# Performance work log

Measured on AMD Instinct MI355X. Metric: run time of the kernel, lower is better.

## Reference

```python
import jax, jax.numpy as jnp
import numpy as np

D_MODEL = 1024
NHEAD = 16
HEAD_DIM = D_MODEL // NHEAD
B, T = 2, 2048


def setup_inputs() -> dict:
    key = jax.random.key(0)
    ks = jax.random.split(key, 12)
    s = 1.0 / np.sqrt(D_MODEL)
    return {
        "query": jax.random.normal(ks[0], (B, T, D_MODEL), jnp.float32),
        "key": jax.random.normal(ks[1], (B, T, D_MODEL), jnp.float32),
        "value": jax.random.normal(ks[2], (B, T, D_MODEL), jnp.float32),
        "key_padding_mask": jnp.zeros((B, T), dtype=bool),
        "attn_mask": jnp.zeros((T, T), jnp.float32),
        "stoich_frac": jax.random.uniform(ks[3], (B, T), jnp.float32),
        "Wq": jax.random.uniform(ks[4], (D_MODEL, D_MODEL), jnp.float32, -s, s),
        "bq": jnp.zeros((D_MODEL,), jnp.float32),
        "Wk": jax.random.uniform(ks[5], (D_MODEL, D_MODEL), jnp.float32, -s, s),
        "bk": jnp.zeros((D_MODEL,), jnp.float32),
        "Wv": jax.random.uniform(ks[6], (D_MODEL, D_MODEL), jnp.float32, -s, s),
        "bv": jnp.zeros((D_MODEL,), jnp.float32),
        "Wo": jax.random.uniform(ks[7], (D_MODEL, D_MODEL), jnp.float32, -s, s),
        "bo": jnp.zeros((D_MODEL,), jnp.float32),
        "stoich_alpha": jnp.float32(0.1),
    }


def reference(query, key, value, key_padding_mask, attn_mask, stoich_frac,
              Wq, bq, Wk, bk, Wv, bv, Wo, bo, stoich_alpha):
    Bq, Tq, _ = query.shape
    Tk = key.shape[1]
    scale = HEAD_DIM ** -0.5
    # Linear projections (torch Linear: x @ W.T + b), reshape to [B, H, T, Dh]
    Q = (query @ Wq.T + bq).reshape(Bq, Tq, NHEAD, HEAD_DIM).transpose(0, 2, 1, 3)
    K = (key @ Wk.T + bk).reshape(Bq, Tk, NHEAD, HEAD_DIM).transpose(0, 2, 1, 3)
    V = (value @ Wv.T + bv).reshape(Bq, Tk, NHEAD, HEAD_DIM).transpose(0, 2, 1, 3)
    # Scores [B, H, Tq, Tk]
    scores = jnp.einsum("bhqd,bhkd->bhqk", Q, K) * scale
    # Stoichiometric pairwise bias (T_q == T_k path)
    diff = stoich_frac[:, :, None] - stoich_frac[:, None, :]  # [B, Tq, Tk]
    bias = stoich_alpha * (jnp.log1p(jnp.abs(diff)) * jnp.sign(diff))
    scores = scores + bias[:, None, :, :]
    scores = scores + attn_mask  # broadcasts [Tq, Tk]
    scores = jnp.where(key_padding_mask[:, None, None, :], -jnp.inf, scores)
    probs = jax.nn.softmax(scores, axis=-1)
    # dropout: eval mode / p=0 -> identity
    out = jnp.einsum("bhqk,bhkd->bhqd", probs, V)
    out = out.transpose(0, 2, 1, 3).reshape(Bq, Tq, D_MODEL)
    return out @ Wo.T + bo
```

## Files before the change

kernel.cpp:

```cpp
#include <hip/hip_runtime.h>
#include <math.h>

typedef __bf16 bf16_t;
typedef __bf16 bf16x8 __attribute__((ext_vector_type(8)));
typedef __bf16 bf16x4 __attribute__((ext_vector_type(4)));
typedef float  f32x4  __attribute__((ext_vector_type(4)));

#define NHEAD 16
#define HDIM 64
#define DMODEL 1024
#define TSEQ 2048

#define SBAR() __builtin_amdgcn_s_barrier()
#define LGKM0() do { asm volatile("s_waitcnt lgkmcnt(0)" ::: "memory"); \
                     __builtin_amdgcn_sched_barrier(0); } while (0)

__device__ __forceinline__ f32x4 mfma16(bf16x8 a, bf16x8 b, f32x4 c) {
  return __builtin_amdgcn_mfma_f32_16x16x32_bf16(a, b, c, 0, 0, 0);
}

__device__ __forceinline__ void gload16(const bf16_t* g, bf16_t* l) {
  __builtin_amdgcn_global_load_lds((const __attribute__((address_space(1))) void*)g,
                                   (__attribute__((address_space(3))) void*)l, 16, 0, 0);
}

__device__ __forceinline__ unsigned pk2(float lo, float hi) {
  unsigned short a = __builtin_bit_cast(unsigned short, (__bf16)lo);
  unsigned short c = __builtin_bit_cast(unsigned short, (__bf16)hi);
  return ((unsigned)c << 16) | a;
}

__device__ __forceinline__ void cvtstore(f32x4 x0, f32x4 x1, bf16_t* dh, bf16_t* dl, int off) {
  bf16x8 hfr, lfr;
#pragma unroll
  for (int j = 0; j < 4; ++j) {
    float v = x0[j];
    __bf16 hb = (__bf16)v;
    hfr[j] = hb; lfr[j] = (__bf16)(v - (float)hb);
    float w = x1[j];
    __bf16 wb = (__bf16)w;
    hfr[4 + j] = wb; lfr[4 + j] = (__bf16)(w - (float)wb);
  }
  *(bf16x8*)(dh + off) = hfr;
  *(bf16x8*)(dl + off) = lfr;
}

__global__ __launch_bounds__(256)
void build_bias(const float* __restrict__ amask, const unsigned char* __restrict__ kpm,
                const float* __restrict__ sf, const float* __restrict__ alpha_p,
                bf16_t* __restrict__ BM) {
  size_t idx = (size_t)blockIdx.x * 256 + threadIdx.x;
  int k8 = (int)(idx & (TSEQ / 8 - 1));
  size_t bq = idx >> 8;
  int b = (int)(bq >> 11);
  int q = (int)(bq & (TSEQ - 1));
  const float sfq = sf[bq];
  const float alpha = *alpha_p;
  const float* sfk = sf + (size_t)b * TSEQ + k8 * 8;
  const float* am  = amask + (size_t)q * TSEQ + k8 * 8;
  const unsigned char* kp = kpm + (size_t)b * TSEQ + k8 * 8;
  bf16x8 o;
#pragma unroll
  for (int j = 0; j < 8; ++j) {
    float df = sfq - sfk[j];
    float v = alpha * copysignf(log1pf(fabsf(df)), df) + am[j];
    if (kp[j]) v = -1.0e30f;
    o[j] = (__bf16)v;
  }
  *(bf16x8*)&BM[idx * 8] = o;
}

template<int MODE>
__global__ __launch_bounds__(512)
void gemm_mfma(const float* __restrict__ A, const float* __restrict__ W,
               const float* __restrict__ bias,
               bf16_t* __restrict__ obh, bf16_t* __restrict__ obl,
               float* __restrict__ of) {
  __shared__ bf16_t AH[8 * 512], AL[8 * 512], WH[4 * 512], WL[4 * 512];
  const int tid = threadIdx.x;
  const int lane = tid & 63;
  const int a15 = lane & 15, g = lane >> 4;
  const int wv = tid >> 6, wm = wv >> 1, wn = wv & 1;
  const int m0 = blockIdx.y * 128, n0 = blockIdx.x * 64;
  f32x4 acc[2][2] = {};

  const int t0 = tid >> 6, l0 = tid & 63;
  const float* pA0 = A + (size_t)(m0 + t0 * 16 + (l0 & 15)) * DMODEL + 8 * (l0 >> 4);
  const bool doW = (tid < 256);
  const int sW = tid & 255;
  const int tw = sW >> 6, lw = sW & 63;
  const float* pW = W + (size_t)(n0 + tw * 16 + (lw & 15)) * DMODEL + 8 * (lw >> 4);

  f32x4 rA0a = *(const f32x4*)pA0, rA0b = *(const f32x4*)(pA0 + 4);
  f32x4 rWa = {}, rWb = {};
  if (doW) { rWa = *(const f32x4*)pW; rWb = *(const f32x4*)(pW + 4); }

  for (int k0 = 0; k0 < DMODEL; k0 += 32) {
    SBAR();
    cvtstore(rA0a, rA0b, AH, AL, tid * 8);
    if (doW) cvtstore(rWa, rWb, WH, WL, sW * 8);
    __builtin_amdgcn_sched_barrier(0);
    if (k0 + 32 < DMODEL) {
      pA0 += 32;
      rA0a = *(const f32x4*)pA0; rA0b = *(const f32x4*)(pA0 + 4);
      if (doW) { pW += 32; rWa = *(const f32x4*)pW; rWb = *(const f32x4*)(pW + 4); }
    }
    LGKM0();
    SBAR();

    bf16x8 ah[2], al[2], wh[2], wl[2];
#pragma unroll
    for (int i = 0; i < 2; ++i) {
      ah[i] = *(const bf16x8*)&AH[(wm * 2 + i) * 512 + lane * 8];
      al[i] = *(const bf16x8*)&AL[(wm * 2 + i) * 512 + lane * 8];
      wh[i] = *(const bf16x8*)&WH[(wn * 2 + i) * 512 + lane * 8];
      wl[i] = *(const bf16x8*)&WL[(wn * 2 + i) * 512 + lane * 8];
    }
    __builtin_amdgcn_s_setprio(1);
    if (MODE == 2) {
#pragma unroll
      for (int i = 0; i < 2; ++i)
#pragma unroll
        for (int j = 0; j < 2; ++j) {
          acc[i][j] = mfma16(wh[i], ah[j], acc[i][j]);
          acc[i][j] = mfma16(wh[i], al[j], acc[i][j]);
          acc[i][j] = mfma16(wl[i], ah[j], acc[i][j]);
        }
    } else {
#pragma unroll
      for (int i = 0; i < 2; ++i)
#pragma unroll
        for (int j = 0; j < 2; ++j) {
          acc[i][j] = mfma16(ah[i], wh[j], acc[i][j]);
          acc[i][j] = mfma16(ah[i], wl[j], acc[i][j]);
          acc[i][j] = mfma16(al[i], wh[j], acc[i][j]);
        }
    }
    __builtin_amdgcn_s_setprio(0);
  }

  if (MODE == 0) {
#pragma unroll
    for (int i = 0; i < 2; ++i)
#pragma unroll
      for (int j = 0; j < 2; ++j) {
        int n = n0 + wn * 32 + j * 16 + a15;
        float bs = bias[n];
#pragma unroll
        for (int r = 0; r < 4; ++r) {
          int m = m0 + wm * 32 + i * 16 + 4 * g + r;
          of[(size_t)m * DMODEL + n] = acc[i][j][r] + bs;
        }
      }
  } else if (MODE == 1) {
#pragma unroll
    for (int i = 0; i < 2; ++i)
#pragma unroll
      for (int j = 0; j < 2; ++j) {
        int n = n0 + wn * 32 + j * 16 + a15;
        float bs = bias[n];
        int hh = n >> 6, d = n & 63;
#pragma unroll
        for (int r = 0; r < 4; ++r) {
          int m = m0 + wm * 32 + i * 16 + 4 * g + r;
          int bb = m >> 11, t = m & (TSEQ - 1);
          float v = acc[i][j][r] + bs;
          size_t o = (((size_t)(bb * NHEAD + hh)) * TSEQ + t) * HDIM + d;
          __bf16 hb = (__bf16)v;
          obh[o] = hb;
          obl[o] = (__bf16)(v - (float)hb);
        }
      }
  } else {
#pragma unroll
    for (int i = 0; i < 2; ++i)
#pragma unroll
      for (int j = 0; j < 2; ++j) {
        int m = m0 + wm * 32 + j * 16 + a15;
        int bb = m >> 11, t = m & (TSEQ - 1);
#pragma unroll
        for (int r = 0; r < 4; ++r) {
          int n = n0 + wn * 32 + i * 16 + 4 * g + r;
          float v = acc[i][j][r] + bias[n];
          int hh = n >> 6, d = n & 63;
          size_t o = (((size_t)(bb * NHEAD + hh)) * HDIM + d) * TSEQ + t;
          __bf16 hb = (__bf16)v;
          obh[o] = hb;
          obl[o] = (__bf16)(v - (float)hb);
        }
      }
  }
}

__global__ __launch_bounds__(512)
void attn_mfma(const bf16_t* __restrict__ Qhi, const bf16_t* __restrict__ Qlo,
               const bf16_t* __restrict__ Khi, const bf16_t* __restrict__ Klo,
               const bf16_t* __restrict__ Vth, const bf16_t* __restrict__ Vtl,
               const bf16_t* __restrict__ BMt, float* __restrict__ O) {
  __shared__ bf16_t KH[2][8 * 512], KL[2][8 * 512], VH[2][8 * 512], VL[2][8 * 512];
  __shared__ bf16_t PS[8 * 512];
  const int tid = threadIdx.x;
  const int lane = tid & 63, wv = tid >> 6;
  const int a15 = lane & 15, g = lane >> 4;
  const int b = blockIdx.z, h = blockIdx.y, q0 = blockIdx.x * 128;
  const int bh = b * NHEAD + h;
  const int qg = q0 + wv * 16 + a15;
  constexpr int NT = TSEQ / 64;

  const bf16_t* Qh_b = Qhi + ((size_t)bh * TSEQ + qg) * HDIM;
  const bf16_t* Ql_b = Qlo + ((size_t)bh * TSEQ + qg) * HDIM;
  const bf16_t* Kh_b = Khi + (size_t)bh * TSEQ * HDIM;
  const bf16_t* Kl_b = Klo + (size_t)bh * TSEQ * HDIM;
  const bf16_t* Vh_b = Vth + (size_t)bh * HDIM * TSEQ;
  const bf16_t* Vl_b = Vtl + (size_t)bh * HDIM * TSEQ;
  const bf16_t* bmrow = BMt + ((size_t)b * TSEQ + qg) * TSEQ;

  bf16x8 qh[2], ql[2];
  qh[0] = *(const bf16x8*)&Qh_b[8 * g];
  qh[1] = *(const bf16x8*)&Qh_b[32 + 8 * g];
  ql[0] = *(const bf16x8*)&Ql_b[8 * g];
  ql[1] = *(const bf16x8*)&Ql_b[32 + 8 * g];

  f32x4 aco[4] = {};
  float m_run = -3.0e38f, l_run = 0.f;
  bf16x4 bmv[4], bmn[4];

  const int ts = wv >> 1, ks = wv & 1;
  auto stage = [&](int k0, int buf) {
    size_t ko = (size_t)(k0 + 16 * ts + a15) * HDIM + 32 * ks + 8 * g;
    gload16(Kh_b + ko, &KH[buf][wv * 512]);
    gload16(Kl_b + ko, &KL[buf][wv * 512]);
    size_t vo = (size_t)(16 * ts + a15) * TSEQ + k0 + 32 * ks + 8 * g;
    gload16(Vh_b + vo, &VH[buf][wv * 512]);
    gload16(Vl_b + vo, &VL[buf][wv * 512]);
  };

#pragma unroll
  for (int mt = 0; mt < 4; ++mt) bmv[mt] = *(const bf16x4*)&bmrow[16 * mt + 4 * g];
  stage(0, 0);

  for (int t = 0; t < NT; ++t) {
    const int cur = t & 1;
    if (t + 1 < NT) {
      const int kn = (t + 1) * 64;
#pragma unroll
      for (int mt = 0; mt < 4; ++mt) bmn[mt] = *(const bf16x4*)&bmrow[kn + 16 * mt + 4 * g];
      stage(kn, cur ^ 1);
      asm volatile("s_waitcnt vmcnt(8)" ::: "memory");
    } else {
      asm volatile("s_waitcnt vmcnt(0)" ::: "memory");
    }
    __builtin_amdgcn_sched_barrier(0);
    SBAR();

    f32x4 s4[4];
    __builtin_amdgcn_s_setprio(1);
#pragma unroll
    for (int mt = 0; mt < 4; ++mt) {
      bf16x8 k0h = *(const bf16x8*)&KH[cur][(mt * 2 + 0) * 512 + lane * 8];
      bf16x8 k1h = *(const bf16x8*)&KH[cur][(mt * 2 + 1) * 512 + lane * 8];
      bf16x8 k0l = *(const bf16x8*)&KL[cur][(mt * 2 + 0) * 512 + lane * 8];
      bf16x8 k1l = *(const bf16x8*)&KL[cur][(mt * 2 + 1) * 512 + lane * 8];
      f32x4 sa = {};
      sa = mfma16(k0h, qh[0], sa);
      sa = mfma16(k1h, qh[1], sa);
      sa = mfma16(k0h, ql[0], sa);
      sa = mfma16(k1h, ql[1], sa);
      sa = mfma16(k0l, qh[0], sa);
      sa = mfma16(k1l, qh[1], sa);
      s4[mt] = sa;
    }
    __builtin_amdgcn_s_setprio(0);

#pragma unroll
    for (int mt = 0; mt < 4; ++mt)
#pragma unroll
      for (int r = 0; r < 4; ++r)
        s4[mt][r] = fmaf(s4[mt][r], 0.125f, (float)bmv[mt][r]);

    float tmax = -3.0e38f;
#pragma unroll
    for (int mt = 0; mt < 4; ++mt)
#pragma unroll
      for (int r = 0; r < 4; ++r) tmax = fmaxf(tmax, s4[mt][r]);
    tmax = fmaxf(tmax, __shfl_xor(tmax, 16));
    tmax = fmaxf(tmax, __shfl_xor(tmax, 32));
    if (!__all(tmax - m_run <= 8.0f)) {
      float mnew = fmaxf(m_run, tmax);
      float corr = __expf(m_run - mnew);
      l_run *= corr;
#pragma unroll
      for (int dt = 0; dt < 4; ++dt) aco[dt] *= corr;
      m_run = mnew;
    }
    float psum = 0.f;
    unsigned pk01[4], pk23[4];
#pragma unroll
    for (int mt = 0; mt < 4; ++mt) {
      float p0 = __expf(s4[mt][0] - m_run);
      float p1 = __expf(s4[mt][1] - m_run);
      float p2 = __expf(s4[mt][2] - m_run);
      float p3 = __expf(s4[mt][3] - m_run);
      psum += (p0 + p1) + (p2 + p3);
      pk01[mt] = pk2(p0, p1);
      pk23[mt] = pk2(p2, p3);
    }
    psum += __shfl_xor(psum, 16);
    psum += __shfl_xor(psum, 32);
    l_run += psum;

    const int psb = wv * 512 + a15 * 32;
    const int r3 = a15 & 3;
    __builtin_amdgcn_s_setprio(1);
#pragma unroll
    for (int kss = 0; kss < 2; ++kss) {
#pragma unroll
      for (int mh = 0; mh < 2; ++mh) {
        int mt = kss * 2 + mh;
        int phys = ((mh << 1) | (g >> 1)) ^ r3;
        uint2 w2;
        w2.x = pk01[mt];
        w2.y = pk23[mt];
        *(uint2*)&PS[psb + phys * 8 + (g & 1) * 4] = w2;
      }
      LGKM0();
      bf16x8 pf = *(const bf16x8*)&PS[psb + ((g ^ r3) << 3)];
#pragma unroll
      for (int dt = 0; dt < 4; ++dt) {
        bf16x8 vh = *(const bf16x8*)&VH[cur][(dt * 2 + kss) * 512 + lane * 8];
        bf16x8 vl = *(const bf16x8*)&VL[cur][(dt * 2 + kss) * 512 + lane * 8];
        aco[dt] = mfma16(vh, pf, aco[dt]);
        aco[dt] = mfma16(vl, pf, aco[dt]);
      }
    }
    __builtin_amdgcn_s_setprio(0);

    if (t + 1 < NT) {
#pragma unroll
      for (int mt = 0; mt < 4; ++mt) bmv[mt] = bmn[mt];
    }
    SBAR();
  }

  float inv = 1.0f / l_run;
#pragma unroll
  for (int dt = 0; dt < 4; ++dt) {
    f32x4 o = aco[dt] * inv;
    *(f32x4*)&O[((size_t)b * TSEQ + qg) * DMODEL + h * HDIM + dt * 16 + 4 * g] = o;
  }
}

extern "C" void kernel_launch(void* const* d_in, const int* in_sizes, int n_in,
                              void* d_out, int out_size, void* d_ws, size_t ws_size,
                              hipStream_t stream) {
  const float* query = (const float*)d_in[0];
  const float* key = (const float*)d_in[1];
  const float* value = (const float*)d_in[2];
  const unsigned char* kpm = (const unsigned char*)d_in[3];
  const float* amask = (const float*)d_in[4];
  const float* sf = (const float*)d_in[5];
  const float* Wq = (const float*)d_in[6];
  const float* bq = (const float*)d_in[7];
  const float* Wk = (const float*)d_in[8];
  const float* bk = (const float*)d_in[9];
  const float* Wv = (const float*)d_in[10];
  const float* bv = (const float*)d_in[11];
  const float* Wo = (const float*)d_in[12];
  const float* bo = (const float*)d_in[13];
  const float* alpha = (const float*)d_in[14];
  float* out = (float*)d_out;

  const size_t NEL = (size_t)2 * NHEAD * TSEQ * HDIM;
  bf16_t* p = (bf16_t*)d_ws;
  bf16_t* Qh = p;
  bf16_t* Ql = p + NEL;
  bf16_t* Kh = p + 2 * NEL;
  bf16_t* Kl = p + 3 * NEL;
  bf16_t* Vh = p + 4 * NEL;
  bf16_t* Vl = p + 5 * NEL;
  float* Oa = (float*)(p + 6 * NEL);
  bf16_t* BMt = (bf16_t*)(Oa + (size_t)4096 * DMODEL);

  build_bias<<<dim3(4096), dim3(256), 0, stream>>>(amask, kpm, sf, alpha, BMt);

  dim3 gg(16, 32), gb(512);
  gemm_mfma<1><<<gg, gb, 0, stream>>>(query, Wq, bq, Qh, Ql, nullptr);
  gemm_mfma<1><<<gg, gb, 0, stream>>>(key, Wk, bk, Kh, Kl, nullptr);
  gemm_mfma<2><<<gg, gb, 0, stream>>>(value, Wv, bv, Vh, Vl, nullptr);
  dim3 ga(TSEQ / 128, NHEAD, 2);
  attn_mfma<<<ga, dim3(512), 0, stream>>>(Qh, Ql, Kh, Kl, Vh, Vl, BMt, Oa);
  gemm_mfma<0><<<gg, gb, 0, stream>>>(Oa, Wo, bo, nullptr, nullptr, out);
}
```

Measured before the change: 338.7 us.

## Process two 16-row query tiles per wave in attention, halving block threads

The attention kernel moves from 8 waves with one 16-query tile each to 4 waves with two 16-query tiles each (A and B), still 128 queries per block. Each K/V fragment read from LDS now feeds twice the MFMA work, which cuts LDS traffic per FLOP, and each wave stages two chunks of K/V. The bias prefetch now happens after the softmax instead of being double-buffered at the loop top. In exchange, per-thread register pressure roughly doubles (two accumulator sets, two score sets, two Q fragments) and there are half as many waves to hide latency.

```diff
diff --git a/kernel.cpp b/kernel.cpp
--- a/kernel.cpp
+++ b/kernel.cpp
@@ -192,60 +192,72 @@
   }
 }
 
-__global__ __launch_bounds__(512)
+__global__ __launch_bounds__(256)
 void attn_mfma(const bf16_t* __restrict__ Qhi, const bf16_t* __restrict__ Qlo,
                const bf16_t* __restrict__ Khi, const bf16_t* __restrict__ Klo,
                const bf16_t* __restrict__ Vth, const bf16_t* __restrict__ Vtl,
                const bf16_t* __restrict__ BMt, float* __restrict__ O) {
   __shared__ bf16_t KH[2][8 * 512], KL[2][8 * 512], VH[2][8 * 512], VL[2][8 * 512];
-  __shared__ bf16_t PS[8 * 512];
+  __shared__ bf16_t PS[4 * 2 * 512];
   const int tid = threadIdx.x;
   const int lane = tid & 63, wv = tid >> 6;
   const int a15 = lane & 15, g = lane >> 4;
   const int b = blockIdx.z, h = blockIdx.y, q0 = blockIdx.x * 128;
   const int bh = b * NHEAD + h;
-  const int qg = q0 + wv * 16 + a15;
+  const int qgA = q0 + wv * 32 + a15;
   constexpr int NT = TSEQ / 64;
 
-  const bf16_t* Qh_b = Qhi + ((size_t)bh * TSEQ + qg) * HDIM;
-  const bf16_t* Ql_b = Qlo + ((size_t)bh * TSEQ + qg) * HDIM;
+  const bf16_t* QhA = Qhi + ((size_t)bh * TSEQ + qgA) * HDIM;
+  const bf16_t* QlA = Qlo + ((size_t)bh * TSEQ + qgA) * HDIM;
   const bf16_t* Kh_b = Khi + (size_t)bh * TSEQ * HDIM;
   const bf16_t* Kl_b = Klo + (size_t)bh * TSEQ * HDIM;
   const bf16_t* Vh_b = Vth + (size_t)bh * HDIM * TSEQ;
   const bf16_t* Vl_b = Vtl + (size_t)bh * HDIM * TSEQ;
-  const bf16_t* bmrow = BMt + ((size_t)b * TSEQ + qg) * TSEQ;
-
-  bf16x8 qh[2], ql[2];
-  qh[0] = *(const bf16x8*)&Qh_b[8 * g];
-  qh[1] = *(const bf16x8*)&Qh_b[32 + 8 * g];
-  ql[0] = *(const bf16x8*)&Ql_b[8 * g];
-  ql[1] = *(const bf16x8*)&Ql_b[32 + 8 * g];
-
-  f32x4 aco[4] = {};
-  float m_run = -3.0e38f, l_run = 0.f;
-  bf16x4 bmv[4], bmn[4];
-
-  const int ts = wv >> 1, ks = wv & 1;
+  const bf16_t* bmA = BMt + ((size_t)b * TSEQ + qgA) * TSEQ;
+  const bf16_t* bmB = bmA + (size_t)16 * TSEQ;
+
+  bf16x8 qhA[2], qlA[2], qhB[2], qlB[2];
+  qhA[0] = *(const bf16x8*)&QhA[8 * g];
+  qhA[1] = *(const bf16x8*)&QhA[32 + 8 * g];
+  qlA[0] = *(const bf16x8*)&QlA[8 * g];
+  qlA[1] = *(const bf16x8*)&QlA[32 + 8 * g];
+  qhB[0] = *(const bf16x8*)&QhA[16 * HDIM + 8 * g];
+  qhB[1] = *(const bf16x8*)&QhA[16 * HDIM + 32 + 8 * g];
+  qlB[0] = *(const bf16x8*)&QlA[16 * HDIM + 8 * g];
+  qlB[1] = *(const bf16x8*)&QlA[16 * HDIM + 32 + 8 * g];
+
+  f32x4 acoA[4] = {}, acoB[4] = {};
+  float mA = -3.0e38f, lA = 0.f, mB = -3.0e38f, lB = 0.f;
+  bf16x4 bmvA[4], bmvB[4];
+
   auto stage = [&](int k0, int buf) {
-    size_t ko = (size_t)(k0 + 16 * ts + a15) * HDIM + 32 * ks + 8 * g;
-    gload16(Kh_b + ko, &KH[buf][wv * 512]);
-    gload16(Kl_b + ko, &KL[buf][wv * 512]);
-    size_t vo = (size_t)(16 * ts + a15) * TSEQ + k0 + 32 * ks + 8 * g;
-    gload16(Vh_b + vo, &VH[buf][wv * 512]);
-    gload16(Vl_b + vo, &VL[buf][wv * 512]);
+#pragma unroll
+    for (int c = 0; c < 2; ++c) {
+      int sb = wv * 2 + c;
+      size_t ko = (size_t)(k0 + 16 * wv + a15) * HDIM + 32 * c + 8 * g;
+      gload16(Kh_b + ko, &KH[buf][sb * 512]);
+      gload16(Kl_b + ko, &KL[buf][sb * 512]);
+      size_t vo = (size_t)(16 * wv + a15) * TSEQ + k0 + 32 * c + 8 * g;
+      gload16(Vh_b + vo, &VH[buf][sb * 512]);
+      gload16(Vl_b + vo, &VL[buf][sb * 512]);
+    }
   };
 
 #pragma unroll
-  for (int mt = 0; mt < 4; ++mt) bmv[mt] = *(const bf16x4*)&bmrow[16 * mt + 4 * g];
+  for (int mt = 0; mt < 4; ++mt) {
+    bmvA[mt] = *(const bf16x4*)&bmA[16 * mt + 4 * g];
+    bmvB[mt] = *(const bf16x4*)&bmB[16 * mt + 4 * g];
+  }
   stage(0, 0);
+
+  const int psbA = (wv * 2 + 0) * 512 + a15 * 32;
+  const int psbB = (wv * 2 + 1) * 512 + a15 * 32;
+  const int r3 = a15 & 3;
 
   for (int t = 0; t < NT; ++t) {
     const int cur = t & 1;
     if (t + 1 < NT) {
-      const int kn = (t + 1) * 64;
-#pragma unroll
-      for (int mt = 0; mt < 4; ++mt) bmn[mt] = *(const bf16x4*)&bmrow[kn + 16 * mt + 4 * g];
-      stage(kn, cur ^ 1);
+      stage((t + 1) * 64, cur ^ 1);
       asm volatile("s_waitcnt vmcnt(8)" ::: "memory");
     } else {
       asm volatile("s_waitcnt vmcnt(0)" ::: "memory");
@@ -253,7 +265,7 @@
     __builtin_amdgcn_sched_barrier(0);
     SBAR();
 
-    f32x4 s4[4];
+    f32x4 s4a[4], s4b[4];
     __builtin_amdgcn_s_setprio(1);
 #pragma unroll
     for (int mt = 0; mt < 4; ++mt) {
@@ -262,13 +274,21 @@
       bf16x8 k0l = *(const bf16x8*)&KL[cur][(mt * 2 + 0) * 512 + lane * 8];
       bf16x8 k1l = *(const bf16x8*)&KL[cur][(mt * 2 + 1) * 512 + lane * 8];
       f32x4 sa = {};
-      sa = mfma16(k0h, qh[0], sa);
-      sa = mfma16(k1h, qh[1], sa);
-      sa = mfma16(k0h, ql[0], sa);
-      sa = mfma16(k1h, ql[1], sa);
-      sa = mfma16(k0l, qh[0], sa);
-      sa = mfma16(k1l, qh[1], sa);
-      s4[mt] = sa;
+      sa = mfma16(k0h, qhA[0], sa);
+      sa = mfma16(k1h, qhA[1], sa);
+      sa = mfma16(k0h, qlA[0], sa);
+      sa = mfma16(k1h, qlA[1], sa);
+      sa = mfma16(k0l, qhA[0], sa);
+      sa = mfma16(k1l, qhA[1], sa);
+      s4a[mt] = sa;
+      f32x4 sb_ = {};
+      sb_ = mfma16(k0h, qhB[0], sb_);
+      sb_ = mfma16(k1h, qhB[1], sb_);
+      sb_ = mfma16(k0h, qlB[0], sb_);
+      sb_ = mfma16(k1h, qlB[1], sb_);
+      sb_ = mfma16(k0l, qhB[0], sb_);
+      sb_ = mfma16(k1l, qhB[1], sb_);
+      s4b[mt] = sb_;
     }
     __builtin_amdgcn_s_setprio(0);
 
@@ -276,41 +296,83 @@
     for (int mt = 0; mt < 4; ++mt)
 #pragma unroll
       for (int r = 0; r < 4; ++r)
-        s4[mt][r] = fmaf(s4[mt][r], 0.125f, (float)bmv[mt][r]);
-
-    float tmax = -3.0e38f;
+        s4a[mt][r] = fmaf(s4a[mt][r], 0.125f, (float)bmvA[mt][r]);
+    float tmaxA = -3.0e38f;
 #pragma unroll
     for (int mt = 0; mt < 4; ++mt)
 #pragma unroll
-      for (int r = 0; r < 4; ++r) tmax = fmaxf(tmax, s4[mt][r]);
-    tmax = fmaxf(tmax, __shfl_xor(tmax, 16));
-    tmax = fmaxf(tmax, __shfl_xor(tmax, 32));
-    if (!__all(tmax - m_run <= 8.0f)) {
-      float mnew = fmaxf(m_run, tmax);
-      float corr = __expf(m_run - mnew);
-      l_run *= corr;
-#pragma unroll
-      for (int dt = 0; dt < 4; ++dt) aco[dt] *= corr;
-      m_run = mnew;
-    }
-    float psum = 0.f;
-    unsigned pk01[4], pk23[4];
+      for (int r = 0; r < 4; ++r) tmaxA = fmaxf(tmaxA, s4a[mt][r]);
+    tmaxA = fmaxf(tmaxA, __shfl_xor(tmaxA, 16));
+    tmaxA = fmaxf(tmaxA, __shfl_xor(tmaxA, 32));
+    if (!__all(tmaxA - mA <= 8.0f)) {
+      float mn = fmaxf(mA, tmaxA);
+      float corr = __expf(mA - mn);
+      lA *= corr;
+#pragma unroll
+      for (int dt = 0; dt < 4; ++dt) acoA[dt] *= corr;
+      mA = mn;
+    }
+    float psumA = 0.f;
+    unsigned pk01A[4], pk23A[4];
 #pragma unroll
     for (int mt = 0; mt < 4; ++mt) {
-      float p0 = __expf(s4[mt][0] - m_run);
-      float p1 = __expf(s4[mt][1] - m_run);
-      float p2 = __expf(s4[mt][2] - m_run);
-      float p3 = __expf(s4[mt][3] - m_run);
-      psum += (p0 + p1) + (p2 + p3);
-      pk01[mt] = pk2(p0, p1);
-      pk23[mt] = pk2(p2, p3);
-    }
-    psum += __shfl_xor(psum, 16);
-    psum += __shfl_xor(psum, 32);
-    l_run += psum;
-
-    const int psb = wv * 512 + a15 * 32;
-    const int r3 = a15 & 3;
+      float p0 = __expf(s4a[mt][0] - mA);
+      float p1 = __expf(s4a[mt][1] - mA);
+      float p2 = __expf(s4a[mt][2] - mA);
+      float p3 = __expf(s4a[mt][3] - mA);
+      psumA += (p0 + p1) + (p2 + p3);
+      pk01A[mt] = pk2(p0, p1);
+      pk23A[mt] = pk2(p2, p3);
+    }
+    psumA += __shfl_xor(psumA, 16);
+    psumA += __shfl_xor(psumA, 32);
+    lA += psumA;
+
+#pragma unroll
+    for (int mt = 0; mt < 4; ++mt)
+#pragma unroll
+      for (int r = 0; r < 4; ++r)
+        s4b[mt][r] = fmaf(s4b[mt][r], 0.125f, (float)bmvB[mt][r]);
+    float tmaxB = -3.0e38f;
+#pragma unroll
+    for (int mt = 0; mt < 4; ++mt)
+#pragma unroll
+      for (int r = 0; r < 4; ++r) tmaxB = fmaxf(tmaxB, s4b[mt][r]);
+    tmaxB = fmaxf(tmaxB, __shfl_xor(tmaxB, 16));
+    tmaxB = fmaxf(tmaxB, __shfl_xor(tmaxB, 32));
+    if (!__all(tmaxB - mB <= 8.0f)) {
+      float mn = fmaxf(mB, tmaxB);
+      float corr = __expf(mB - mn);
+      lB *= corr;
+#pragma unroll
+      for (int dt = 0; dt < 4; ++dt) acoB[dt] *= corr;
+      mB = mn;
+    }
+    float psumB = 0.f;
+    unsigned pk01B[4], pk23B[4];
+#pragma unroll
+    for (int mt = 0; mt < 4; ++mt) {
+      float p0 = __expf(s4b[mt][0] - mB);
+      float p1 = __expf(s4b[mt][1] - mB);
+      float p2 = __expf(s4b[mt][2] - mB);
+      float p3 = __expf(s4b[mt][3] - mB);
+      psumB += (p0 + p1) + (p2 + p3);
+      pk01B[mt] = pk2(p0, p1);
+      pk23B[mt] = pk2(p2, p3);
+    }
+    psumB += __shfl_xor(psumB, 16);
+    psumB += __shfl_xor(psumB, 32);
+    lB += psumB;
+
+    if (t + 1 < NT) {
+      const int kn = (t + 1) * 64;
+#pragma unroll
+      for (int mt = 0; mt < 4; ++mt) {
+        bmvA[mt] = *(const bf16x4*)&bmA[kn + 16 * mt + 4 * g];
+        bmvB[mt] = *(const bf16x4*)&bmB[kn + 16 * mt + 4 * g];
+      }
+    }
+
     __builtin_amdgcn_s_setprio(1);
 #pragma unroll
     for (int kss = 0; kss < 2; ++kss) {
@@ -318,35 +380,36 @@
       for (int mh = 0; mh < 2; ++mh) {
         int mt = kss * 2 + mh;
         int phys = ((mh << 1) | (g >> 1)) ^ r3;
-        uint2 w2;
-        w2.x = pk01[mt];
-        w2.y = pk23[mt];
-        *(uint2*)&PS[psb + phys * 8 + (g & 1) * 4] = w2;
+        uint2 wA; wA.x = pk01A[mt]; wA.y = pk23A[mt];
+        *(uint2*)&PS[psbA + phys * 8 + (g & 1) * 4] = wA;
+        uint2 wB; wB.x = pk01B[mt]; wB.y = pk23B[mt];
+        *(uint2*)&PS[psbB + phys * 8 + (g & 1) * 4] = wB;
       }
       LGKM0();
-      bf16x8 pf = *(const bf16x8*)&PS[psb + ((g ^ r3) << 3)];
+      bf16x8 pfA = *(const bf16x8*)&PS[psbA + ((g ^ r3) << 3)];
+      bf16x8 pfB = *(const bf16x8*)&PS[psbB + ((g ^ r3) << 3)];
 #pragma unroll
       for (int dt = 0; dt < 4; ++dt) {
         bf16x8 vh = *(const bf16x8*)&VH[cur][(dt * 2 + kss) * 512 + lane * 8];
         bf16x8 vl = *(const bf16x8*)&VL[cur][(dt * 2 + kss) * 512 + lane * 8];
-        aco[dt] = mfma16(vh, pf, aco[dt]);
-        aco[dt] = mfma16(vl, pf, aco[dt]);
+        acoA[dt] = mfma16(vh, pfA, acoA[dt]);
+        acoA[dt] = mfma16(vl, pfA, acoA[dt]);
+        acoB[dt] = mfma16(vh, pfB, acoB[dt]);
+        acoB[dt] = mfma16(vl, pfB, acoB[dt]);
       }
     }
     __builtin_amdgcn_s_setprio(0);
 
-    if (t + 1 < NT) {
-#pragma unroll
-      for (int mt = 0; mt < 4; ++mt) bmv[mt] = bmn[mt];
-    }
     SBAR();
   }
 
-  float inv = 1.0f / l_run;
+  float invA = 1.0f / lA, invB = 1.0f / lB;
 #pragma unroll
   for (int dt = 0; dt < 4; ++dt) {
-    f32x4 o = aco[dt] * inv;
-    *(f32x4*)&O[((size_t)b * TSEQ + qg) * DMODEL + h * HDIM + dt * 16 + 4 * g] = o;
+    f32x4 oA = acoA[dt] * invA;
+    *(f32x4*)&O[((size_t)b * TSEQ + qgA) * DMODEL + h * HDIM + dt * 16 + 4 * g] = oA;
+    f32x4 oB = acoB[dt] * invB;
+    *(f32x4*)&O[((size_t)b * TSEQ + qgA + 16) * DMODEL + h * HDIM + dt * 16 + 4 * g] = oB;
   }
 }
 
@@ -388,6 +451,6 @@
   gemm_mfma<1><<<gg, gb, 0, stream>>>(key, Wk, bk, Kh, Kl, nullptr);
   gemm_mfma<2><<<gg, gb, 0, stream>>>(value, Wv, bv, Vh, Vl, nullptr);
   dim3 ga(TSEQ / 128, NHEAD, 2);
-  attn_mfma<<<ga, dim3(512), 0, stream>>>(Qh, Ql, Kh, Kl, Vh, Vl, BMt, Oa);
+  attn_mfma<<<ga, dim3(256), 0, stream>>>(Qh, Ql, Kh, Kl, Vh, Vl, BMt, Oa);
   gemm_mfma<0><<<gg, gb, 0, stream>>>(Oa, Wo, bo, nullptr, nullptr, out);
 }
```

After: 355.0 us. 1.05x slower.

## Pre-split weights to bf16 hi/lo and stream them via async LDS loads

Applied to the files above, without the earlier changes.

Adds a kernel that converts all four fp32 weight matrices into bf16 high/low halves once per call. The QKV GEMMs then load the pre-split weights straight into double-buffered LDS with global_load_lds, instead of converting them in registers on every k-step. The attention kernel now writes its output as bf16 hi/lo pairs, so the output projection can stream both operands with async LDS loads and skip per-tile conversion. The cost is an extra launch and extra weight traffic for the split, plus more workspace.

```diff
diff --git a/kernel.cpp b/kernel.cpp
--- a/kernel.cpp
+++ b/kernel.cpp
@@ -10,8 +10,10 @@
 #define HDIM 64
 #define DMODEL 1024
 #define TSEQ 2048
+#define WEL (DMODEL * DMODEL)
 
 #define SBAR() __builtin_amdgcn_s_barrier()
+#define SCHED0() __builtin_amdgcn_sched_barrier(0)
 #define LGKM0() do { asm volatile("s_waitcnt lgkmcnt(0)" ::: "memory"); \
                      __builtin_amdgcn_sched_barrier(0); } while (0)
 
@@ -43,6 +45,28 @@
   }
   *(bf16x8*)(dh + off) = hfr;
   *(bf16x8*)(dl + off) = lfr;
+}
+
+__global__ __launch_bounds__(256)
+void presplit_w(const float* __restrict__ w0, const float* __restrict__ w1,
+                const float* __restrict__ w2, const float* __restrict__ w3,
+                bf16_t* __restrict__ out) {
+  const int y = blockIdx.y;
+  const float* src = (y == 0) ? w0 : (y == 1) ? w1 : (y == 2) ? w2 : w3;
+  size_t i = ((size_t)blockIdx.x * 256 + threadIdx.x) * 8;
+  f32x4 a = *(const f32x4*)(src + i);
+  f32x4 c = *(const f32x4*)(src + i + 4);
+  bf16x8 h, l;
+#pragma unroll
+  for (int j = 0; j < 4; ++j) {
+    __bf16 hb = (__bf16)a[j];
+    h[j] = hb; l[j] = (__bf16)(a[j] - (float)hb);
+    __bf16 cb = (__bf16)c[j];
+    h[4 + j] = cb; l[4 + j] = (__bf16)(c[j] - (float)cb);
+  }
+  bf16_t* dh = out + (size_t)y * 2 * WEL;
+  *(bf16x8*)(dh + i) = h;
+  *(bf16x8*)(dh + WEL + i) = l;
 }
 
 __global__ __launch_bounds__(256)
@@ -72,11 +96,10 @@
 
 template<int MODE>
 __global__ __launch_bounds__(512)
-void gemm_mfma(const float* __restrict__ A, const float* __restrict__ W,
-               const float* __restrict__ bias,
-               bf16_t* __restrict__ obh, bf16_t* __restrict__ obl,
-               float* __restrict__ of) {
-  __shared__ bf16_t AH[8 * 512], AL[8 * 512], WH[4 * 512], WL[4 * 512];
+void gemm_qkv(const float* __restrict__ A, const bf16_t* __restrict__ Wh,
+              const bf16_t* __restrict__ Wl, const float* __restrict__ bias,
+              bf16_t* __restrict__ obh, bf16_t* __restrict__ obl) {
+  __shared__ bf16_t AH[8 * 512], AL[8 * 512], WHs[2][4 * 512], WLs[2][4 * 512];
   const int tid = threadIdx.x;
   const int lane = tid & 63;
   const int a15 = lane & 15, g = lane >> 4;
@@ -85,25 +108,29 @@
   f32x4 acc[2][2] = {};
 
   const int t0 = tid >> 6, l0 = tid & 63;
-  const float* pA0 = A + (size_t)(m0 + t0 * 16 + (l0 & 15)) * DMODEL + 8 * (l0 >> 4);
-  const bool doW = (tid < 256);
-  const int sW = tid & 255;
-  const int tw = sW >> 6, lw = sW & 63;
-  const float* pW = W + (size_t)(n0 + tw * 16 + (lw & 15)) * DMODEL + 8 * (lw >> 4);
-
-  f32x4 rA0a = *(const f32x4*)pA0, rA0b = *(const f32x4*)(pA0 + 4);
-  f32x4 rWa = {}, rWb = {};
-  if (doW) { rWa = *(const f32x4*)pW; rWb = *(const f32x4*)(pW + 4); }
-
-  for (int k0 = 0; k0 < DMODEL; k0 += 32) {
-    SBAR();
-    cvtstore(rA0a, rA0b, AH, AL, tid * 8);
-    if (doW) cvtstore(rWa, rWb, WH, WL, sW * 8);
-    __builtin_amdgcn_sched_barrier(0);
-    if (k0 + 32 < DMODEL) {
-      pA0 += 32;
-      rA0a = *(const f32x4*)pA0; rA0b = *(const f32x4*)(pA0 + 4);
-      if (doW) { pW += 32; rWa = *(const f32x4*)pW; rWb = *(const f32x4*)(pW + 4); }
+  const float* pA = A + (size_t)(m0 + t0 * 16 + (l0 & 15)) * DMODEL + 8 * (l0 >> 4);
+  const int wts = wv & 3;
+  const bf16_t* pWg = ((wv < 4) ? Wh : Wl) + (size_t)(n0 + wts * 16 + a15) * DMODEL + 8 * g;
+
+  f32x4 rAa = *(const f32x4*)pA, rAb = *(const f32x4*)(pA + 4);
+  gload16(pWg, (wv < 4) ? &WHs[0][wts * 512] : &WLs[0][wts * 512]);
+
+  constexpr int NK = DMODEL / 32;
+  for (int t = 0; t < NK; ++t) {
+    const int cur = t & 1;
+    SBAR();
+    cvtstore(rAa, rAb, AH, AL, tid * 8);
+    SCHED0();
+    if (t + 1 < NK) {
+      pA += 32;
+      rAa = *(const f32x4*)pA; rAb = *(const f32x4*)(pA + 4);
+      SCHED0();
+      gload16(pWg + (t + 1) * 32, (wv < 4) ? &WHs[cur ^ 1][wts * 512]
+                                           : &WLs[cur ^ 1][wts * 512]);
+      SCHED0();
+      asm volatile("s_waitcnt vmcnt(3)" ::: "memory");
+    } else {
+      asm volatile("s_waitcnt vmcnt(0)" ::: "memory");
     }
     LGKM0();
     SBAR();
@@ -113,8 +140,8 @@
     for (int i = 0; i < 2; ++i) {
       ah[i] = *(const bf16x8*)&AH[(wm * 2 + i) * 512 + lane * 8];
       al[i] = *(const bf16x8*)&AL[(wm * 2 + i) * 512 + lane * 8];
-      wh[i] = *(const bf16x8*)&WH[(wn * 2 + i) * 512 + lane * 8];
-      wl[i] = *(const bf16x8*)&WL[(wn * 2 + i) * 512 + lane * 8];
+      wh[i] = *(const bf16x8*)&WHs[cur][(wn * 2 + i) * 512 + lane * 8];
+      wl[i] = *(const bf16x8*)&WLs[cur][(wn * 2 + i) * 512 + lane * 8];
     }
     __builtin_amdgcn_s_setprio(1);
     if (MODE == 2) {
@@ -139,20 +166,7 @@
     __builtin_amdgcn_s_setprio(0);
   }
 
-  if (MODE == 0) {
-#pragma unroll
-    for (int i = 0; i < 2; ++i)
-#pragma unroll
-      for (int j = 0; j < 2; ++j) {
-        int n = n0 + wn * 32 + j * 16 + a15;
-        float bs = bias[n];
-#pragma unroll
-        for (int r = 0; r < 4; ++r) {
-          int m = m0 + wm * 32 + i * 16 + 4 * g + r;
-          of[(size_t)m * DMODEL + n] = acc[i][j][r] + bs;
-        }
-      }
-  } else if (MODE == 1) {
+  if (MODE == 1) {
 #pragma unroll
     for (int i = 0; i < 2; ++i)
 #pragma unroll
@@ -193,10 +207,82 @@
 }
 
 __global__ __launch_bounds__(512)
+void gemm_out(const bf16_t* __restrict__ Ah, const bf16_t* __restrict__ Al,
+              const bf16_t* __restrict__ Wh, const bf16_t* __restrict__ Wl,
+              const float* __restrict__ bias, float* __restrict__ of) {
+  __shared__ bf16_t AHs[2][8 * 512], ALs[2][8 * 512], WHs[2][4 * 512], WLs[2][4 * 512];
+  const int tid = threadIdx.x;
+  const int lane = tid & 63;
+  const int a15 = lane & 15, g = lane >> 4;
+  const int wv = tid >> 6, wm = wv >> 1, wn = wv & 1;
+  const int m0 = blockIdx.y * 128, n0 = blockIdx.x * 64;
+  f32x4 acc[2][2] = {};
+
+  const bf16_t* pAh = Ah + (size_t)(m0 + wv * 16 + a15) * DMODEL + 8 * g;
+  const bf16_t* pAl = Al + (size_t)(m0 + wv * 16 + a15) * DMODEL + 8 * g;
+  const int wts = wv & 3;
+  const bf16_t* pWg = ((wv < 4) ? Wh : Wl) + (size_t)(n0 + wts * 16 + a15) * DMODEL + 8 * g;
+
+  auto stage = [&](int t, int buf) {
+    gload16(pAh + t * 32, &AHs[buf][wv * 512]);
+    gload16(pAl + t * 32, &ALs[buf][wv * 512]);
+    gload16(pWg + t * 32, (wv < 4) ? &WHs[buf][wts * 512] : &WLs[buf][wts * 512]);
+  };
+  stage(0, 0);
+
+  constexpr int NK = DMODEL / 32;
+  for (int t = 0; t < NK; ++t) {
+    const int cur = t & 1;
+    if (t + 1 < NK) {
+      stage(t + 1, cur ^ 1);
+      asm volatile("s_waitcnt vmcnt(3)" ::: "memory");
+    } else {
+      asm volatile("s_waitcnt vmcnt(0)" ::: "memory");
+    }
+    SCHED0();
+    SBAR();
+
+    bf16x8 ah[2], al[2], wh[2], wl[2];
+#pragma unroll
+    for (int i = 0; i < 2; ++i) {
+      ah[i] = *(const bf16x8*)&AHs[cur][(wm * 2 + i) * 512 + lane * 8];
+      al[i] = *(const bf16x8*)&ALs[cur][(wm * 2 + i) * 512 + lane * 8];
+      wh[i] = *(const bf16x8*)&WHs[cur][(wn * 2 + i) * 512 + lane * 8];
+      wl[i] = *(const bf16x8*)&WLs[cur][(wn * 2 + i) * 512 + lane * 8];
+    }
+    __builtin_amdgcn_s_setprio(1);
+#pragma unroll
+    for (int i = 0; i < 2; ++i)
+#pragma unroll
+      for (int j = 0; j < 2; ++j) {
+        acc[i][j] = mfma16(ah[i], wh[j], acc[i][j]);
+        acc[i][j] = mfma16(ah[i], wl[j], acc[i][j]);
+        acc[i][j] = mfma16(al[i], wh[j], acc[i][j]);
+      }
+    __builtin_amdgcn_s_setprio(0);
+    SBAR();
+  }
+
+#pragma unroll
+  for (int i = 0; i < 2; ++i)
+#pragma unroll
+    for (int j = 0; j < 2; ++j) {
+      int n = n0 + wn * 32 + j * 16 + a15;
+      float bs = bias[n];
+#pragma unroll
+      for (int r = 0; r < 4; ++r) {
+        int m = m0 + wm * 32 + i * 16 + 4 * g + r;
+        of[(size_t)m * DMODEL + n] = acc[i][j][r] + bs;
+      }
+    }
+}
+
+__global__ __launch_bounds__(512)
 void attn_mfma(const bf16_t* __restrict__ Qhi, const bf16_t* __restrict__ Qlo,
                const bf16_t* __restrict__ Khi, const bf16_t* __restrict__ Klo,
                const bf16_t* __restrict__ Vth, const bf16_t* __restrict__ Vtl,
-               const bf16_t* __restrict__ BMt, float* __restrict__ O) {
+               const bf16_t* __restrict__ BMt,
+               bf16_t* __restrict__ Oh, bf16_t* __restrict__ Ol) {
   __shared__ bf16_t KH[2][8 * 512], KL[2][8 * 512], VH[2][8 * 512], VL[2][8 * 512];
   __shared__ bf16_t PS[8 * 512];
   const int tid = threadIdx.x;
@@ -239,6 +325,9 @@
   for (int mt = 0; mt < 4; ++mt) bmv[mt] = *(const bf16x4*)&bmrow[16 * mt + 4 * g];
   stage(0, 0);
 
+  const int psb = wv * 512 + a15 * 32;
+  const int r3 = a15 & 3;
+
   for (int t = 0; t < NT; ++t) {
     const int cur = t & 1;
     if (t + 1 < NT) {
@@ -250,7 +339,7 @@
     } else {
       asm volatile("s_waitcnt vmcnt(0)" ::: "memory");
     }
-    __builtin_amdgcn_sched_barrier(0);
+    SCHED0();
     SBAR();
 
     f32x4 s4[4];
@@ -309,8 +398,6 @@
     psum += __shfl_xor(psum, 32);
     l_run += psum;
 
-    const int psb = wv * 512 + a15 * 32;
-    const int r3 = a15 & 3;
     __builtin_amdgcn_s_setprio(1);
 #pragma unroll
     for (int kss = 0; kss < 2; ++kss) {
@@ -346,7 +433,16 @@
 #pragma unroll
   for (int dt = 0; dt < 4; ++dt) {
     f32x4 o = aco[dt] * inv;
-    *(f32x4*)&O[((size_t)b * TSEQ + qg) * DMODEL + h * HDIM + dt * 16 + 4 * g] = o;
+    bf16x4 oh, ol;
+#pragma unroll
+    for (int r = 0; r < 4; ++r) {
+      __bf16 hb = (__bf16)o[r];
+      oh[r] = hb;
+      ol[r] = (__bf16)(o[r] - (float)hb);
+    }
+    size_t off = ((size_t)b * TSEQ + qg) * DMODEL + h * HDIM + dt * 16 + 4 * g;
+    *(bf16x4*)&Oh[off] = oh;
+    *(bf16x4*)&Ol[off] = ol;
   }
 }
 
@@ -378,16 +474,23 @@
   bf16_t* Kl = p + 3 * NEL;
   bf16_t* Vh = p + 4 * NEL;
   bf16_t* Vl = p + 5 * NEL;
-  float* Oa = (float*)(p + 6 * NEL);
-  bf16_t* BMt = (bf16_t*)(Oa + (size_t)4096 * DMODEL);
-
+  bf16_t* Oh = p + 6 * NEL;
+  bf16_t* Ol = p + 7 * NEL;
+  bf16_t* BMt = p + 8 * NEL;
+  bf16_t* wsp = p + 10 * NEL;
+  bf16_t* wqh = wsp + 0 * WEL, *wql = wsp + 1 * WEL;
+  bf16_t* wkh = wsp + 2 * WEL, *wkl = wsp + 3 * WEL;
+  bf16_t* wvh = wsp + 4 * WEL, *wvl = wsp + 5 * WEL;
+  bf16_t* woh = wsp + 6 * WEL, *wol = wsp + 7 * WEL;
+
+  presplit_w<<<dim3(WEL / (256 * 8), 4), dim3(256), 0, stream>>>(Wq, Wk, Wv, Wo, wsp);
   build_bias<<<dim3(4096), dim3(256), 0, stream>>>(amask, kpm, sf, alpha, BMt);
 
   dim3 gg(16, 32), gb(512);
-  gemm_mfma<1><<<gg, gb, 0, stream>>>(query, Wq, bq, Qh, Ql, nullptr);
-  gemm_mfma<1><<<gg, gb, 0, stream>>>(key, Wk, bk, Kh, Kl, nullptr);
-  gemm_mfma<2><<<gg, gb, 0, stream>>>(value, Wv, bv, Vh, Vl, nullptr);
+  gemm_qkv<1><<<gg, gb, 0, stream>>>(query, wqh, wql, bq, Qh, Ql);
+  gemm_qkv<1><<<gg, gb, 0, stream>>>(key, wkh, wkl, bk, Kh, Kl);
+  gemm_qkv<2><<<gg, gb, 0, stream>>>(value, wvh, wvl, bv, Vh, Vl);
   dim3 ga(TSEQ / 128, NHEAD, 2);
-  attn_mfma<<<ga, dim3(512), 0, stream>>>(Qh, Ql, Kh, Kl, Vh, Vl, BMt, Oa);
-  gemm_mfma<0><<<gg, gb, 0, stream>>>(Oa, Wo, bo, nullptr, nullptr, out);
-}
+  attn_mfma<<<ga, gb, 0, stream>>>(Qh, Ql, Kh, Kl, Vh, Vl, BMt, Oh, Ol);
+  gemm_out<<<gg, gb, 0, stream>>>(Oh, Ol, woh, wol, bo, out);
+}
```

New measurement: 347.2 us. +2.5%, slower.
